# Kernel tuning notes

Hardware: AMD Instinct MI355X
Metric: run time of the kernel (lower is better)

The kernel has to match this reference:

```python
import jax, jax.numpy as jnp
import numpy as np

SCALE = 2
R_MAX = 3
ALPHA_DYN = 2.0
NEG_INF = -1e9
EPS_SIG = 1e-6

HL = WL = DL = 32
HH = WH = DH = 64
C_FEAT = 32
G_GUIDE = 3


def setup_inputs() -> dict:
    key = jax.random.key(0)
    k = jax.random.split(key, 6)
    feat_lr = jax.random.normal(k[0], (1, C_FEAT, HL, WL, DL), jnp.float32)
    guide_hr = jax.random.normal(k[1], (1, G_GUIDE, HH, WH, DH), jnp.float32)
    log_s = float(np.log(1.5))
    log_sr = float(np.log(0.1))
    sx_raw = log_s + 0.05 * jax.random.normal(k[2], (1, 1, HL, WL, DL), jnp.float32)
    sy_raw = log_s + 0.05 * jax.random.normal(k[3], (1, 1, HL, WL, DL), jnp.float32)
    sz_raw = log_s + 0.05 * jax.random.normal(k[4], (1, 1, HL, WL, DL), jnp.float32)
    sr_raw = log_sr + 0.05 * jax.random.normal(k[5], (1, 1, HL, WL, DL), jnp.float32)
    return {"feat_lr": feat_lr, "guide_hr": guide_hr, "sx_raw": sx_raw,
            "sy_raw": sy_raw, "sz_raw": sz_raw, "sr_raw": sr_raw}


def _resize3(x, shape):
    # F.interpolate(mode='trilinear', align_corners=False) == half-pixel linear resize
    return jax.image.resize(x, shape, method='trilinear')


def reference(feat_lr, guide_hr, sx_raw, sy_raw, sz_raw, sr_raw):
    C, Hl, Wl, Dl = feat_lr.shape[1:]
    G, Hh, Wh, Dh = guide_hr.shape[1:]
    feat = feat_lr[0].astype(jnp.float32)          # [C,Hl,Wl,Dl]
    guide = guide_hr[0].astype(jnp.float32)        # [G,Hh,Wh,Dh]
    # sigma maps (exp of learnable log-sigmas), clamp_min applied on maps (== on gathers)
    sx = jnp.maximum(jnp.exp(sx_raw[0, 0]), EPS_SIG)   # [Hl,Wl,Dl]
    sy = jnp.maximum(jnp.exp(sy_raw[0, 0]), EPS_SIG)
    sz = jnp.maximum(jnp.exp(sz_raw[0, 0]), EPS_SIG)
    sr = jnp.maximum(jnp.exp(sr_raw[0, 0]), EPS_SIG)

    x = jnp.arange(Hh, dtype=jnp.float32)
    y = jnp.arange(Wh, dtype=jnp.float32)
    z = jnp.arange(Dh, dtype=jnp.float32)
    X, Y, Z = jnp.meshgrid(x, y, z, indexing='ij')    # [Hh,Wh,Dh]
    u = (X + 0.5) / SCALE - 0.5
    v = (Y + 0.5) / SCALE - 0.5
    w_ = (Z + 0.5) / SCALE - 0.5
    uc = jnp.clip(jnp.round(u), 0, Hl - 1).astype(jnp.int32)
    vc = jnp.clip(jnp.round(v), 0, Wl - 1).astype(jnp.int32)
    wc = jnp.clip(jnp.round(w_), 0, Dl - 1).astype(jnp.int32)

    sigma_eff = jnp.maximum(sx, jnp.maximum(sy, sz))
    sigma_eff_hr = _resize3(sigma_eff, (Hh, Wh, Dh))
    R_map = jnp.clip(jnp.ceil(ALPHA_DYN * sigma_eff_hr), 1.0, float(R_MAX))  # [Hh,Wh,Dh]
    R2 = R_map * R_map

    guide_lr = _resize3(guide, (G, Hl, Wl, Dl))        # [G,Hl,Wl,Dl]

    offs = np.arange(-R_MAX, R_MAX + 1)
    dXg, dYg, dZg = np.meshgrid(offs, offs, offs, indexing='ij')
    offsets = jnp.asarray(np.stack([dXg.ravel(), dYg.ravel(), dZg.ravel()], 1),
                          dtype=jnp.int32)            # [343,3]

    num0 = jnp.zeros((C, Hh, Wh, Dh), jnp.float32)
    den0 = jnp.zeros((Hh, Wh, Dh), jnp.float32)
    m0 = jnp.full((Hh, Wh, Dh), NEG_INF, jnp.float32)

    def step(carry, off):
        num, den, m = carry
        dX, dY, dZ = off[0], off[1], off[2]
        Ui = jnp.clip(uc + dX, 0, Hl - 1)              # [Hh,Wh,Dh]
        Vi = jnp.clip(vc + dY, 0, Wl - 1)
        Wi = jnp.clip(wc + dZ, 0, Dl - 1)
        r2 = (dX * dX + dY * dY + dZ * dZ).astype(jnp.float32)
        mask = r2 <= R2
        cx = (Ui.astype(jnp.float32) + 0.5) * SCALE - 0.5
        cy = (Vi.astype(jnp.float32) + 0.5) * SCALE - 0.5
        cz = (Wi.astype(jnp.float32) + 0.5) * SCALE - 0.5
        dx = X - cx
        dy = Y - cy
        dz = Z - cz
        sxg = sx[Ui, Vi, Wi]
        syg = sy[Ui, Vi, Wi]
        szg = sz[Ui, Vi, Wi]
        srg = sr[Ui, Vi, Wi]
        log_ws = -dx * dx / (2 * sxg * sxg) - dy * dy / (2 * syg * syg) - dz * dz / (2 * szg * szg)
        g0 = guide_lr[:, Ui, Vi, Wi]                   # [G,Hh,Wh,Dh]
        diff2 = jnp.sum((guide - g0) ** 2, axis=0)
        log_wr = -diff2 / (2 * srg * srg + 1e-8)
        log_w = jnp.where(mask, log_ws + log_wr, NEG_INF)
        # online log-sum-exp merge (flash-attention style)
        m_new = jnp.maximum(m, log_w)
        scale_old = jnp.exp(m - m_new)
        wgt = jnp.exp(log_w - m_new)
        f = feat[:, Ui, Vi, Wi]                        # [C,Hh,Wh,Dh]
        num = num * scale_old + f * wgt
        den = den * scale_old + wgt
        return (num, den, m_new), None

    (num, den, _), _ = jax.lax.scan(step, (num0, den0, m0), offsets)
    out = (num / jnp.maximum(den, 1e-8))[None]         # [1,C,Hh,Wh,Dh]
    return out.astype(feat_lr.dtype)
```

## Files before the change

### kernel.cpp

```cpp
#include <hip/hip_runtime.h>

typedef float f32x2 __attribute__((ext_vector_type(2)));
typedef _Float16 h2 __attribute__((ext_vector_type(2)));

constexpr float LOG2E = 1.4426950408889634f;
#define TBIG 3.0e38f
#define PD 38
#define PD2 1444
#define NPC 54872

struct Ent { int e0; int r2; float fx, fy, fz; int dxi, dyi, dzi; };
struct Tabs { Ent e[2][62]; };
constexpr Tabs make_tabs() {
    int dxs[123], dys[123], dzs[123]; int n = 0;
    for (int rr = 0; rr <= 9; ++rr)
        for (int a = -3; a <= 3; ++a)
            for (int b = -3; b <= 3; ++b)
                for (int c = -3; c <= 3; ++c)
                    if (a*a + b*b + c*c == rr) { dxs[n]=a; dys[n]=b; dzs[n]=c; ++n; }
    Tabs T{};
    for (int p = 0; p < 2; ++p)
        for (int j = 0; j < 62; ++j) {
            int k = 2*j + p;
            if (k < 123) {
                int a = dxs[k], b = dys[k], c = dzs[k];
                int tci = (a*PD + b)*PD + c;
                T.e[p][j].e0 = tci*32;
                T.e[p][j].r2 = a*a + b*b + c*c;
                T.e[p][j].fx = 2.f*a; T.e[p][j].fy = 2.f*b; T.e[p][j].fz = 2.f*c;
                T.e[p][j].dxi = a; T.e[p][j].dyi = b; T.e[p][j].dzi = c;
            } else {
                T.e[p][j].e0 = 0; T.e[p][j].r2 = 999;
            }
        }
    return T;
}
__constant__ Tabs TB = make_tabs();

__device__ __forceinline__ float fast_exp2(float x) { return __builtin_amdgcn_exp2f(x); }

__device__ __forceinline__ void mk_taps(int j, int idx[4], float wt[4]) {
    float s = 0.f;
#pragma unroll
    for (int k = 0; k < 4; ++k) {
        int i = 2*j - 1 + k;
        float w = (k == 0 || k == 3) ? 0.25f : 0.75f;
        bool ok = (i >= 0) && (i < 64);
        wt[k] = ok ? w : 0.f;
        idx[k] = ok ? i : 0;
        s += wt[k];
    }
    float inv = 1.f / s;
#pragma unroll
    for (int k = 0; k < 4; ++k) wt[k] *= inv;
}

__global__ void prepABpad(const float* __restrict__ sxr, const float* __restrict__ syr,
                          const float* __restrict__ szr, const float* __restrict__ srr,
                          const float* __restrict__ guide,
                          float4* __restrict__ param4, float* __restrict__ sigEff) {
    int t = blockIdx.x * 256 + threadIdx.x;
    if (t >= NPC) return;
    int pu = t / PD2; int rem = t - pu*PD2; int pv = rem / PD; int pw = rem - pv*PD;
    int u = min(max(pu-3, 0), 31), v = min(max(pv-3, 0), 31), w = min(max(pw-3, 0), 31);
    int ci = (u*32 + v)*32 + w;
    float sx = fmaxf(expf(sxr[ci]), 1e-6f);
    float sy = fmaxf(expf(syr[ci]), 1e-6f);
    float sz = fmaxf(expf(szr[ci]), 1e-6f);
    float sr = fmaxf(expf(srr[ci]), 1e-6f);
    param4[2*t] = make_float4(0.5f/(sx*sx), 0.5f/(sy*sy), 0.5f/(sz*sz), 1.0f/(2.0f*sr*sr + 1e-8f));
    if (pu-3 == u && pv-3 == v && pw-3 == w) sigEff[ci] = fmaxf(sx, fmaxf(sy, sz));

    int iu[4], iv[4], iw[4];
    float wu[4], wv[4], ww[4];
    mk_taps(u, iu, wu); mk_taps(v, iv, wv); mk_taps(w, iw, ww);
    float g0 = 0.f, g1 = 0.f, g2 = 0.f;
#pragma unroll
    for (int a = 0; a < 4; ++a)
#pragma unroll
        for (int b = 0; b < 4; ++b) {
            float wab = wu[a]*wv[b];
            int base = iu[a]*4096 + iv[b]*64;
#pragma unroll
            for (int c = 0; c < 4; ++c) {
                float wt = wab*ww[c];
                int gi = base + iw[c];
                g0 += wt*guide[gi];
                g1 += wt*guide[262144 + gi];
                g2 += wt*guide[524288 + gi];
            }
        }
    param4[2*t + 1] = make_float4(g0, g1, g2, 0.f);
}

__global__ void prepTpad(const float* __restrict__ feat, _Float16* __restrict__ featH) {
    __shared__ float tile[32][33];
    int uv = blockIdx.x;
    int u = uv >> 5, v = uv & 31;
    int col = threadIdx.x & 31;
    int row = threadIdx.x >> 5;
#pragma unroll
    for (int it = 0; it < 4; ++it) {
        int c = row + it*8;
        tile[c][col] = feat[((c*32 + u)*32 + v)*32 + col];
    }
    __syncthreads();
#pragma unroll
    for (int it = 0; it < 4; ++it) {
        int w = row + it*8;
        int pci = (u+3)*PD2 + (v+3)*PD + (w+3);
        featH[pci*32 + col] = (_Float16)tile[col][w];
    }
}

__global__ void prepBorder(_Float16* __restrict__ featH) {
    int t = blockIdx.x * 256 + threadIdx.x;
    if (t >= NPC) return;
    int pu = t / PD2; int rem = t - pu*PD2; int pv = rem / PD; int pw = rem - pv*PD;
    int u = min(max(pu-3, 0), 31), v = min(max(pv-3, 0), 31), w = min(max(pw-3, 0), 31);
    if (pu-3 == u && pv-3 == v && pw-3 == w) return;
    int src = ((u+3)*PD2 + (v+3)*PD + (w+3))*32;
    uint4* d = (uint4*)(featH + t*32);
    const uint4* s = (const uint4*)(featH + src);
    d[0] = s[0]; d[1] = s[1]; d[2] = s[2]; d[3] = s[3];
}

template<bool INTER>
__device__ __forceinline__ float weight_tt(const char* __restrict__ pb, int voffp,
                                           const Ent& E, int R2i,
                                           int uc, int vc, int wc,
                                           float exf, float eyf, float ezf,
                                           float Xh, float Yh, float Zh,
                                           float G0, float G1, float G2) {
    float4 A  = *(const float4*)(pb + (unsigned)voffp);
    float4 Bv = *(const float4*)(pb + (unsigned)voffp + 16);
    float ddx, ddy, ddz;
    if (INTER) {
        ddx = exf - E.fx;
        ddy = eyf - E.fy;
        ddz = ezf - E.fz;
    } else {
        int Ui = min(max(uc + E.dxi, 0), 31);
        int Vi = min(max(vc + E.dyi, 0), 31);
        int Wi = min(max(wc + E.dzi, 0), 31);
        ddx = fmaf(-2.f, (float)Ui, Xh);
        ddy = fmaf(-2.f, (float)Vi, Yh);
        ddz = fmaf(-2.f, (float)Wi, Zh);
    }
    float tt = fmaf(ddx*ddx, A.x, fmaf(ddy*ddy, A.y, ddz*ddz*A.z));
    float d0 = G0 - Bv.x, d1 = G1 - Bv.y, d2 = G2 - Bv.z;
    tt = fmaf(fmaf(d0, d0, fmaf(d1, d1, d2*d2)), A.w, tt);
    return (E.r2 <= R2i) ? tt : TBIG;
}

template<bool INTER>
__device__ __forceinline__ void run_body(const char* __restrict__ pb, const char* __restrict__ fb,
                                         int par, int jcount, int pbase, int fbase, int R2i,
                                         int uc, int vc, int wc,
                                         float exf, float eyf, float ezf,
                                         float Xh, float Yh, float Zh,
                                         float G0, float G1, float G2,
                                         float* sx_my, const float* sx_oth,
                                         f32x2 (&num2)[4][4], float& den, float& ML) {
    float tmin = TBIG;
#pragma unroll 2
    for (int j = 0; j < jcount; ++j) {
        Ent E = TB.e[par][j];
        int voffp = pbase + E.e0;
        float tt = weight_tt<INTER>(pb, voffp, E, R2i, uc, vc, wc,
                                    exf, eyf, ezf, Xh, Yh, Zh, G0, G1, G2);
        tmin = fminf(tmin, tt);
    }
    *sx_my = tmin;
    __syncthreads();
    tmin = fminf(tmin, *sx_oth);
    ML = tmin * LOG2E;

#pragma unroll 2
    for (int j = 0; j < jcount; ++j) {
        Ent E = TB.e[par][j];
        int voffp = pbase + E.e0;
        int vofff = fbase + E.e0*2;
        float tt = weight_tt<INTER>(pb, voffp, E, R2i, uc, vc, wc,
                                    exf, eyf, ezf, Xh, Yh, Zh, G0, G1, G2);
        float wgt = fast_exp2(fmaf(tt, -LOG2E, ML));
        den += wgt;
        float w1 = __shfl_xor(wgt, 1), w8 = __shfl_xor(wgt, 8), w9 = __shfl_xor(wgt, 9);
        float4 F = *(const float4*)(fb + (unsigned)vofff);
        h2 q0 = __builtin_bit_cast(h2, F.x);
        h2 q1 = __builtin_bit_cast(h2, F.y);
        h2 q2 = __builtin_bit_cast(h2, F.z);
        h2 q3 = __builtin_bit_cast(h2, F.w);
        f32x2 f0 = {(float)q0.x, (float)q0.y};
        f32x2 f1 = {(float)q1.x, (float)q1.y};
        f32x2 f2 = {(float)q2.x, (float)q2.y};
        f32x2 f3 = {(float)q3.x, (float)q3.y};
        f32x2 w0v = {wgt, wgt}, w1v = {w1, w1}, w2v = {w8, w8}, w3v = {w9, w9};
        num2[0][0] += f0*w0v; num2[0][1] += f1*w0v; num2[0][2] += f2*w0v; num2[0][3] += f3*w0v;
        num2[1][0] += f0*w1v; num2[1][1] += f1*w1v; num2[1][2] += f2*w1v; num2[1][3] += f3*w1v;
        num2[2][0] += f0*w2v; num2[2][1] += f1*w2v; num2[2][2] += f2*w2v; num2[2][3] += f3*w2v;
        num2[3][0] += f0*w3v; num2[3][1] += f1*w3v; num2[3][2] += f2*w3v; num2[3][3] += f3*w3v;
    }
}

__global__ __launch_bounds__(256, 4)
void jbu_main(const float* __restrict__ guide, const float4* __restrict__ param4,
              const float* __restrict__ sigEff, const _Float16* __restrict__ featH,
              float* __restrict__ out) {
    __shared__ float mbuf[2][64][33];
    __shared__ float sxch[2][2][64];
    int tid = threadIdx.x;
    int widx = tid >> 6;
    int l = tid & 63;
    int par = __builtin_amdgcn_readfirstlane(widx & 1);
    int q = __builtin_amdgcn_readfirstlane(widx >> 1);
    int bsw = (blockIdx.x & 7) * 256 + (blockIdx.x >> 3);
    int tIdx = bsw * 2 + q;
    int X = __builtin_amdgcn_readfirstlane(tIdx >> 6);
    int Y0 = ((tIdx >> 3) & 7) << 3;
    int Z0 = (tIdx & 7) << 3;
    int y = l >> 3, z = l & 7;
    int Y = Y0 + y, Z = Z0 + z;
    int h = ((y & 1) << 1) | (z & 1);
    int vox = (X << 12) + (Y << 6) + Z;

    float G0 = guide[vox];
    float G1 = guide[262144 + vox];
    float G2 = guide[524288 + vox];

    int x0 = max((X-1) >> 1, 0), x1 = min(((X-1) >> 1) + 1, 31);
    int y0 = max((Y-1) >> 1, 0), y1 = min(((Y-1) >> 1) + 1, 31);
    int z0 = max((Z-1) >> 1, 0), z1 = min(((Z-1) >> 1) + 1, 31);
    float wx1 = (X & 1) ? 0.25f : 0.75f, wx0 = 1.f - wx1;
    float wy1 = (Y & 1) ? 0.25f : 0.75f, wy0 = 1.f - wy1;
    float wz1 = (Z & 1) ? 0.25f : 0.75f, wz0 = 1.f - wz1;
#define SG(i, j, k) sigEff[((i)*32 + (j))*32 + (k)]
    float se =
        wx0*(wy0*(wz0*SG(x0,y0,z0) + wz1*SG(x0,y0,z1)) +
             wy1*(wz0*SG(x0,y1,z0) + wz1*SG(x0,y1,z1))) +
        wx1*(wy0*(wz0*SG(x1,y0,z0) + wz1*SG(x1,y0,z1)) +
             wy1*(wz0*SG(x1,y1,z0) + wz1*SG(x1,y1,z1)));
#undef SG
    float Rf = fminf(fmaxf(ceilf(2.f*se), 1.f), 3.f);
    int R2i = (int)(Rf*Rf + 0.5f);
    bool a9 = __any((int)(R2i >= 9));
    bool a4 = __any((int)(R2i >= 4));
    int nmax = a9 ? 123 : (a4 ? 33 : 7);
    int jcount = __builtin_amdgcn_readfirstlane((nmax - par + 1) >> 1);

    int uc = X >> 1, vc = Y >> 1, wc = Z >> 1;
    float Xh = (float)X - 0.5f, Yh = (float)Y - 0.5f, Zh = (float)Z - 0.5f;
    float exf = (float)(X - 2*uc) - 0.5f;
    float eyf = (float)(Y - 2*vc) - 0.5f;
    float ezf = (float)(Z - 2*wc) - 0.5f;

    int pci = (uc+3)*PD2 + (vc+3)*PD + (wc+3);
    int pbase = pci*32;
    int fbase = pci*64 + h*16;

    int vc0 = Y0 >> 1, wc0 = Z0 >> 1;
    bool inter = (uc >= 3 && uc <= 28 && vc0 >= 3 && vc0 <= 25 && wc0 >= 3 && wc0 <= 25);

    f32x2 num2[4][4];
#pragma unroll
    for (int r = 0; r < 4; ++r)
#pragma unroll
        for (int p = 0; p < 4; ++p) num2[r][p] = {0.f, 0.f};
    float den = 0.f, ML = 0.f;

    const char* pb = (const char*)param4;
    const char* fb = (const char*)featH;
    float* sx_my  = &sxch[q][par][l];
    const float* sx_oth = &sxch[q][par ^ 1][l];

    if (inter)
        run_body<true>(pb, fb, par, jcount, pbase, fbase, R2i, uc, vc, wc,
                       exf, eyf, ezf, Xh, Yh, Zh, G0, G1, G2, sx_my, sx_oth, num2, den, ML);
    else
        run_body<false>(pb, fb, par, jcount, pbase, fbase, R2i, uc, vc, wc,
                        exf, eyf, ezf, Xh, Yh, Zh, G0, G1, G2, sx_my, sx_oth, num2, den, ML);

    float* mp = &mbuf[q][l][0];
    if (par) {
#pragma unroll
        for (int r = 0; r < 4; ++r)
#pragma unroll
            for (int p = 0; p < 4; ++p) {
                mp[r*8 + 2*p]     = num2[r][p].x;
                mp[r*8 + 2*p + 1] = num2[r][p].y;
            }
        mp[32] = den;
    }
    __syncthreads();
    if (par) return;

#pragma unroll
    for (int r = 0; r < 4; ++r)
#pragma unroll
        for (int p = 0; p < 4; ++p) {
            num2[r][p].x += mp[r*8 + 2*p];
            num2[r][p].y += mp[r*8 + 2*p + 1];
        }
    den += mp[32];

    float invd = 1.0f / fmaxf(den, 1e-8f);
    float i1 = __shfl_xor(invd, 1), i8 = __shfl_xor(invd, 8), i9 = __shfl_xor(invd, 9);
    float* ob = out + (size_t)(h*8) * 262144;
#pragma unroll
    for (int p = 0; p < 4; ++p) {
        f32x2 v0 = num2[0][p], v1 = num2[1][p], v2 = num2[2][p], v3 = num2[3][p];
        ob[(2*p)*262144 + vox]          = v0.x * invd;
        ob[(2*p+1)*262144 + vox]        = v0.y * invd;
        ob[(2*p)*262144 + (vox ^ 1)]    = v1.x * i1;
        ob[(2*p+1)*262144 + (vox ^ 1)]  = v1.y * i1;
        ob[(2*p)*262144 + (vox ^ 64)]   = v2.x * i8;
        ob[(2*p+1)*262144 + (vox ^ 64)] = v2.y * i8;
        ob[(2*p)*262144 + (vox ^ 65)]   = v3.x * i9;
        ob[(2*p+1)*262144 + (vox ^ 65)] = v3.y * i9;
    }
}

extern "C" void kernel_launch(void* const* d_in, const int* in_sizes, int n_in,
                              void* d_out, int out_size, void* d_ws, size_t ws_size,
                              hipStream_t stream) {
    const float* feat  = (const float*)d_in[0];
    const float* guide = (const float*)d_in[1];
    const float* sxr = (const float*)d_in[2];
    const float* syr = (const float*)d_in[3];
    const float* szr = (const float*)d_in[4];
    const float* srr = (const float*)d_in[5];
    float* out = (float*)d_out;

    char* ws = (char*)d_ws;
    float4* param4  = (float4*)ws;
    float* sigEff   = (float*)(ws + 2097152);
    _Float16* featH = (_Float16*)(ws + 2228224);

    prepABpad<<<215, 256, 0, stream>>>(sxr, syr, szr, srr, guide, param4, sigEff);
    prepTpad<<<1024, 256, 0, stream>>>(feat, featH);
    prepBorder<<<215, 256, 0, stream>>>(featH);
    jbu_main<<<2048, 256, 0, stream>>>(guide, param4, sigEff, featH, out);
}
```

Measured before the change: 109.5 us.

## Split main kernel into 128-thread blocks and pack tap table entries

Each block now handles one 8x8 tile with two waves (one per parity half) rather than two tiles with four waves, so the launch grows to 4096 blocks of 128 threads and shared memory per block halves. The tap table entry is repacked to 32 bytes, with a precomputed feature offset and the three integer offsets packed into one int, and the table is padded to 64 entries per parity. The two tap loops are unrolled by 4 instead of 2. The aim is to cut barrier coupling between waves, simplify constant loads and expose more memory-level parallelism, at the cost of possible register pressure from the deeper unroll and a different block-to-tile order that may affect cache locality.

```diff
diff --git a/kernel.cpp b/kernel.cpp
--- a/kernel.cpp
+++ b/kernel.cpp
@@ -9,8 +9,8 @@
 #define PD2 1444
 #define NPC 54872
 
-struct Ent { int e0; int r2; float fx, fy, fz; int dxi, dyi, dzi; };
-struct Tabs { Ent e[2][62]; };
+struct Ent { int e0; int e2; int r2; int pk; float fx, fy, fz, pad; };
+struct Tabs { Ent e[2][64]; };
 constexpr Tabs make_tabs() {
     int dxs[123], dys[123], dzs[123]; int n = 0;
     for (int rr = 0; rr <= 9; ++rr)
@@ -20,17 +20,21 @@
                     if (a*a + b*b + c*c == rr) { dxs[n]=a; dys[n]=b; dzs[n]=c; ++n; }
     Tabs T{};
     for (int p = 0; p < 2; ++p)
-        for (int j = 0; j < 62; ++j) {
+        for (int j = 0; j < 64; ++j) {
             int k = 2*j + p;
             if (k < 123) {
                 int a = dxs[k], b = dys[k], c = dzs[k];
                 int tci = (a*PD + b)*PD + c;
                 T.e[p][j].e0 = tci*32;
+                T.e[p][j].e2 = tci*64;
                 T.e[p][j].r2 = a*a + b*b + c*c;
+                T.e[p][j].pk = (a+3) | ((b+3)<<8) | ((c+3)<<16);
                 T.e[p][j].fx = 2.f*a; T.e[p][j].fy = 2.f*b; T.e[p][j].fz = 2.f*c;
-                T.e[p][j].dxi = a; T.e[p][j].dyi = b; T.e[p][j].dzi = c;
+                T.e[p][j].pad = 0.f;
             } else {
-                T.e[p][j].e0 = 0; T.e[p][j].r2 = 999;
+                T.e[p][j].e0 = 0; T.e[p][j].e2 = 0; T.e[p][j].r2 = 999;
+                T.e[p][j].pk = 3 | (3<<8) | (3<<16);
+                T.e[p][j].fx = 0.f; T.e[p][j].fy = 0.f; T.e[p][j].fz = 0.f; T.e[p][j].pad = 0.f;
             }
         }
     return T;
@@ -140,9 +144,9 @@
         ddy = eyf - E.fy;
         ddz = ezf - E.fz;
     } else {
-        int Ui = min(max(uc + E.dxi, 0), 31);
-        int Vi = min(max(vc + E.dyi, 0), 31);
-        int Wi = min(max(wc + E.dzi, 0), 31);
+        int Ui = min(max(uc + ((E.pk & 255) - 3), 0), 31);
+        int Vi = min(max(vc + (((E.pk >> 8) & 255) - 3), 0), 31);
+        int Wi = min(max(wc + ((E.pk >> 16) - 3), 0), 31);
         ddx = fmaf(-2.f, (float)Ui, Xh);
         ddy = fmaf(-2.f, (float)Vi, Yh);
         ddz = fmaf(-2.f, (float)Wi, Zh);
@@ -163,7 +167,7 @@
                                          float* sx_my, const float* sx_oth,
                                          f32x2 (&num2)[4][4], float& den, float& ML) {
     float tmin = TBIG;
-#pragma unroll 2
+#pragma unroll 4
     for (int j = 0; j < jcount; ++j) {
         Ent E = TB.e[par][j];
         int voffp = pbase + E.e0;
@@ -176,11 +180,11 @@
     tmin = fminf(tmin, *sx_oth);
     ML = tmin * LOG2E;
 
-#pragma unroll 2
+#pragma unroll 4
     for (int j = 0; j < jcount; ++j) {
         Ent E = TB.e[par][j];
         int voffp = pbase + E.e0;
-        int vofff = fbase + E.e0*2;
+        int vofff = fbase + E.e2;
         float tt = weight_tt<INTER>(pb, voffp, E, R2i, uc, vc, wc,
                                     exf, eyf, ezf, Xh, Yh, Zh, G0, G1, G2);
         float wgt = fast_exp2(fmaf(tt, -LOG2E, ML));
@@ -203,19 +207,17 @@
     }
 }
 
-__global__ __launch_bounds__(256, 4)
+__global__ __launch_bounds__(128, 4)
 void jbu_main(const float* __restrict__ guide, const float4* __restrict__ param4,
               const float* __restrict__ sigEff, const _Float16* __restrict__ featH,
               float* __restrict__ out) {
-    __shared__ float mbuf[2][64][33];
-    __shared__ float sxch[2][2][64];
+    __shared__ float mbuf[64][33];
+    __shared__ float sxch[2][64];
     int tid = threadIdx.x;
     int widx = tid >> 6;
     int l = tid & 63;
-    int par = __builtin_amdgcn_readfirstlane(widx & 1);
-    int q = __builtin_amdgcn_readfirstlane(widx >> 1);
-    int bsw = (blockIdx.x & 7) * 256 + (blockIdx.x >> 3);
-    int tIdx = bsw * 2 + q;
+    int par = __builtin_amdgcn_readfirstlane(widx);
+    int tIdx = (blockIdx.x & 7) * 512 + (blockIdx.x >> 3);
     int X = __builtin_amdgcn_readfirstlane(tIdx >> 6);
     int Y0 = ((tIdx >> 3) & 7) << 3;
     int Z0 = (tIdx & 7) << 3;
@@ -270,8 +272,8 @@
 
     const char* pb = (const char*)param4;
     const char* fb = (const char*)featH;
-    float* sx_my  = &sxch[q][par][l];
-    const float* sx_oth = &sxch[q][par ^ 1][l];
+    float* sx_my  = &sxch[par][l];
+    const float* sx_oth = &sxch[par ^ 1][l];
 
     if (inter)
         run_body<true>(pb, fb, par, jcount, pbase, fbase, R2i, uc, vc, wc,
@@ -280,7 +282,7 @@
         run_body<false>(pb, fb, par, jcount, pbase, fbase, R2i, uc, vc, wc,
                         exf, eyf, ezf, Xh, Yh, Zh, G0, G1, G2, sx_my, sx_oth, num2, den, ML);
 
-    float* mp = &mbuf[q][l][0];
+    float* mp = &mbuf[l][0];
     if (par) {
 #pragma unroll
         for (int r = 0; r < 4; ++r)
@@ -339,5 +341,5 @@
     prepABpad<<<215, 256, 0, stream>>>(sxr, syr, szr, srr, guide, param4, sigEff);
     prepTpad<<<1024, 256, 0, stream>>>(feat, featH);
     prepBorder<<<215, 256, 0, stream>>>(featH);
-    jbu_main<<<2048, 256, 0, stream>>>(guide, param4, sigEff, featH, out);
-}
+    jbu_main<<<4096, 128, 0, stream>>>(guide, param4, sigEff, featH, out);
+}
```

Result: slower. 126.3 us (+15.4%).
